# Performance work log

Measured on AMD Instinct MI355X. Metric: run time of the kernel, lower is better.

Reference implementation:

```python
import jax, jax.numpy as jnp
import numpy as np

CHANNELS = 256
REDUCTION = 4
REDUCED = max(1, CHANNELS // REDUCTION)  # 64


def setup_inputs() -> dict:
    key = jax.random.key(0)
    kx, kq, kk, kv, ko = jax.random.split(key, 5)
    B, C, H, W = 4, CHANNELS, 48, 48
    x = jax.random.normal(kx, (B, C, H, W), dtype=jnp.float32)
    # 1x1 conv weights (bias=False) for 3 q/k/v branches, stored as [3, reduced, C]
    wq = jax.random.normal(kq, (3, REDUCED, C), dtype=jnp.float32) * 0.05
    wk = jax.random.normal(kk, (3, REDUCED, C), dtype=jnp.float32) * 0.05
    wv = jax.random.normal(kv, (3, REDUCED, C), dtype=jnp.float32) * 0.05
    # output 1x1 conv: [C, 3*reduced]
    wo = jax.random.normal(ko, (C, 3 * REDUCED), dtype=jnp.float32) * 0.05
    return {"x": x, "wq": wq, "wk": wk, "wv": wv, "wo": wo}


def reference(x, wq, wk, wv, wo):
    B, C, H, W = x.shape
    N = H * W
    r = wq.shape[1]
    scale = 1.0 / float(r) ** 0.5
    xf = x.reshape(B, C, N)                      # [B, C, N]
    # 1x1 convs == channel matmuls; all 3 branches at once
    qs = jnp.einsum('irc,bcn->ibrn', wq, xf)     # [3, B, r, N]
    ks = jnp.einsum('irc,bcn->ibrn', wk, xf)
    vs = jnp.einsum('irc,bcn->ibrn', wv, xf)
    outs = []
    for i in range(3):                           # structural 3x3 nesting
        q = qs[i]                                # [B, r, N]
        acc = jnp.zeros((B, r, N), dtype=x.dtype)
        for j in range(3):
            # attn[b, n, m] = softmax_m(q[b,:,n] . k[b,:,m] / sqrt(r))
            attn = jax.nn.softmax(jnp.einsum('brn,brm->bnm', q, ks[j]) * scale, axis=-1)
            acc = acc + jnp.einsum('brm,bnm->brn', vs[j], attn)
        outs.append(acc)
    combined = jnp.concatenate(outs, axis=1)     # [B, 3r, N]
    out = jnp.einsum('cr,brn->bcn', wo, combined).reshape(B, C, H, W)
    return x * jax.nn.sigmoid(out)
```

## Files before the change

kernel.cpp:

```cpp
#include <hip/hip_runtime.h>


#define BB 4
#define CC 256
#define NN_ 2304
#define RR 64

#define OQ 0
#define OK_ 1769472
#define OV 3538944
#define OC 5308416
#define CSTR 1769472
#define FR_IB 147456
#define OXF 10616832
#define OWF 12976128
#define OWOF 13123584

typedef __bf16 bf16x8 __attribute__((ext_vector_type(8)));
typedef float f32x16 __attribute__((ext_vector_type(16)));
typedef unsigned short ushort8 __attribute__((ext_vector_type(8)));
typedef unsigned int uintx2 __attribute__((ext_vector_type(2)));
typedef unsigned int uintx4 __attribute__((ext_vector_type(4)));

#if __has_builtin(__builtin_amdgcn_exp2f)
#define EXP2(x) __builtin_amdgcn_exp2f(x)
#else
#define EXP2(x) exp2f(x)
#endif

__device__ __forceinline__ float bf2f(unsigned short s) {
    unsigned int u = ((unsigned int)s) << 16;
    return __builtin_bit_cast(float, u);
}
__device__ __forceinline__ unsigned int pk_bf16(float lo, float hi) {
    unsigned int r;
    asm("v_cvt_pk_bf16_f32 %0, %1, %2" : "=v"(r) : "v"(lo), "v"(hi));
    return r;
}

__global__ __launch_bounds__(256) void prep_kernel(
    const float* __restrict__ x, const float* __restrict__ wq,
    const float* __restrict__ wk, const float* __restrict__ wv,
    const float* __restrict__ wo, unsigned short* __restrict__ wsb)
{
    int bid = blockIdx.x;
    int t = threadIdx.x;
    if (bid < 9) {
        int s = bid;
        int type = s / 3, i = s % 3;
        const float* wsel = (type == 0) ? wq : (type == 1 ? wk : wv);
        const float scale = (type == 0) ? 0.18033688011112042f : 1.0f;
        unsigned short* dst = wsb + OWF + s * 16384;
        #pragma unroll
        for (int p = 0; p < 8; ++p) {
            int u = t + 256 * p;
            int ks = u >> 7, rb = (u >> 6) & 1, lo = u & 63;
            int row = rb * 32 + (lo & 31), c = ks * 16 + 8 * (lo >> 5);
            const float* src = wsel + ((i * 64 + row) * 256 + c);
            float4 f0 = *(const float4*)(src);
            float4 f1 = *(const float4*)(src + 4);
            uintx4 pwv = {pk_bf16(f0.x * scale, f0.y * scale),
                          pk_bf16(f0.z * scale, f0.w * scale),
                          pk_bf16(f1.x * scale, f1.y * scale),
                          pk_bf16(f1.z * scale, f1.w * scale)};
            *(uintx4*)(dst + (ks * 2 + rb) * 512 + lo * 8) = pwv;
        }
        return;
    }
    if (bid < 12) {
        int bb = bid - 9;
        #pragma unroll
        for (int p = 0; p < 8; ++p) {
            int u = t + 256 * p;
            int cg = bb * 32 + (u >> 6);
            int lane = u & 63;
            int ks = cg >> 3, rb = cg & 7;
            int row = rb * 32 + (lane & 31);
            int g = ks * 16 + 8 * (lane >> 5);
            const float* src = wo + row * 192 + g;
            float4 f0 = *(const float4*)(src);
            float4 f1 = *(const float4*)(src + 4);
            uintx4 pwv = {pk_bf16(f0.x, f0.y), pk_bf16(f0.z, f0.w),
                          pk_bf16(f1.x, f1.y), pk_bf16(f1.z, f1.w)};
            *(uintx4*)(wsb + OWOF + cg * 512 + lane * 8) = pwv;
        }
        return;
    }
    __shared__ __align__(16) float xs[64 * 132];
    int xb = bid - 12;
    int cq  = xb & 3;
    int nt2 = (xb >> 2) % 18;
    int b   = xb / 72;
    int c0 = cq * 64, n0 = nt2 * 128;
    #pragma unroll
    for (int p = 0; p < 8; ++p) {
        int u = t + 256 * p;
        int cl = u >> 5, nq = (u & 31) * 4;
        *(float4*)&xs[cl * 132 + nq] =
            *(const float4*)&x[((size_t)(b * CC + c0 + cl)) * NN_ + n0 + nq];
    }
    __syncthreads();
    unsigned short* xfb = wsb + OXF + ((size_t)b) * 72 * 16 * 512;
    #pragma unroll
    for (int p = 0; p < 4; ++p) {
        int u = t + 256 * p;
        int nb_l = u >> 8, ks_l = (u >> 6) & 3, lo = u & 63;
        int hh = lo >> 5, idx = lo & 31;
        int clb = ks_l * 16 + 8 * hh;
        int nn = nb_l * 32 + idx;
        unsigned int pw[4];
        #pragma unroll
        for (int d = 0; d < 4; ++d) {
            float a  = xs[(clb + 2 * d) * 132 + nn];
            float bb2 = xs[(clb + 2 * d + 1) * 132 + nn];
            pw[d] = pk_bf16(a, bb2);
        }
        int nb = nt2 * 4 + nb_l, ks = cq * 4 + ks_l;
        *(uintx4*)(xfb + (nb * 16 + ks) * 512 + lo * 8) =
            (uintx4){pw[0], pw[1], pw[2], pw[3]};
    }
}

__global__ __launch_bounds__(256) void proj_mfma(unsigned short* __restrict__ wsb)
{
    int bid = blockIdx.x;
    int s = bid / 72;
    int rem = bid % 72;
    int b = rem / 18, nb4 = rem % 18;
    int type = s / 3, i = s % 3;
    int t = threadIdx.x;
    int w = t >> 6, lane = t & 63;
    int lq = lane & 31, h = lane >> 5;
    int nb = nb4 * 4 + w;

    const unsigned short* wf = wsb + OWF + s * 16384 + lane * 8;
    const unsigned short* xf = wsb + OXF + ((size_t)(b * 72 + nb) * 16) * 512 + lane * 8;

    f32x16 o0 = {}, o1 = {};
    if (type < 2) {
        #pragma unroll
        for (int ks = 0; ks < 16; ++ks) {
            bf16x8 a0 = *(const bf16x8*)(wf + ks * 1024);
            bf16x8 a1 = *(const bf16x8*)(wf + ks * 1024 + 512);
            bf16x8 bx = *(const bf16x8*)(xf + ks * 512);
            o0 = __builtin_amdgcn_mfma_f32_32x32x16_bf16(a0, bx, o0, 0, 0, 0);
            o1 = __builtin_amdgcn_mfma_f32_32x32x16_bf16(a1, bx, o1, 0, 0, 0);
        }
    } else {
        #pragma unroll
        for (int ks = 0; ks < 16; ++ks) {
            bf16x8 a0 = *(const bf16x8*)(wf + ks * 1024);
            bf16x8 a1 = *(const bf16x8*)(wf + ks * 1024 + 512);
            bf16x8 bx = *(const bf16x8*)(xf + ks * 512);
            o0 = __builtin_amdgcn_mfma_f32_32x32x16_bf16(bx, a0, o0, 0, 0, 0);
            o1 = __builtin_amdgcn_mfma_f32_32x32x16_bf16(bx, a1, o1, 0, 0, 0);
        }
    }

    unsigned short* dstbase =
        wsb + ((type == 0) ? OQ : (type == 1 ? OK_ : OV)) +
        ((size_t)(i * 4 + b)) * FR_IB + nb * 2048;

    if (type < 2) {
        #pragma unroll
        for (int g = 0; g < 4; ++g) {
            int kd = 8 * g + 4 * h;
            int off = (kd >> 4) * 512 + ((kd >> 3) & 1) * 256 + lq * 8 + (kd & 7);
            *(uintx2*)(dstbase + off) =
                (uintx2){pk_bf16(o0[4 * g], o0[4 * g + 1]),
                         pk_bf16(o0[4 * g + 2], o0[4 * g + 3])};
            int kd2 = kd + 32;
            int off2 = (kd2 >> 4) * 512 + ((kd2 >> 3) & 1) * 256 + lq * 8 + (kd2 & 7);
            *(uintx2*)(dstbase + off2) =
                (uintx2){pk_bf16(o1[4 * g], o1[4 * g + 1]),
                         pk_bf16(o1[4 * g + 2], o1[4 * g + 3])};
        }
    } else {
        #pragma unroll
        for (int g = 0; g < 4; ++g) {
            int off = (g >> 1) * 1024 + (g & 1) * 256 + lq * 8 + 4 * h;
            *(uintx2*)(dstbase + off) =
                (uintx2){pk_bf16(o0[4 * g], o0[4 * g + 1]),
                         pk_bf16(o0[4 * g + 2], o0[4 * g + 3])};
            *(uintx2*)(dstbase + off + 512) =
                (uintx2){pk_bf16(o1[4 * g], o1[4 * g + 1]),
                         pk_bf16(o1[4 * g + 2], o1[4 * g + 3])};
        }
    }
}

__global__ __launch_bounds__(256, 4) void attn_kernel(unsigned short* __restrict__ wsb)
{
    __shared__ __align__(16) float fl[4352];

    int bid = blockIdx.x;
    int wid = (bid & 7) * 162 + (bid >> 3);
    int s12 = wid / 108;
    int rem = wid % 108;
    int j = s12 >> 2, b = s12 & 3;
    int i = rem / 36;
    int qp = rem % 36;
    int w = threadIdx.x >> 6;
    int ks = w & 1, qloc = w >> 1;
    int lane = threadIdx.x & 63;
    int lq = lane & 31;
    int h = lane >> 5;
    int q0 = (qp * 2 + qloc) * 32;
    int nt = q0 >> 5;

    const unsigned short* qtf = wsb + OQ + ((size_t)(i * 4 + b)) * FR_IB +
                                nt * 2048 + lane * 8;
    const unsigned short* kp = wsb + OK_ + ((size_t)(j * 4 + b)) * FR_IB +
                               (size_t)(ks * 36) * 2048 + lane * 8;
    const unsigned short* vp = wsb + OV + ((size_t)(j * 4 + b)) * FR_IB +
                               (size_t)(ks * 36) * 2048 + lane * 8;

    bf16x8 bq0 = *(const bf16x8*)(qtf + 0);
    bf16x8 bq1 = *(const bf16x8*)(qtf + 512);
    bf16x8 bq2 = *(const bf16x8*)(qtf + 1024);
    bf16x8 bq3 = *(const bf16x8*)(qtf + 1536);

    f32x16 o0 = {}, o1 = {};
    float l_loc = 0.f;

    auto compute_step = [&](bf16x8 k0, bf16x8 k1, bf16x8 k2, bf16x8 k3,
                            int step) {
        const unsigned short* vb = vp + (size_t)step * 2048;
        bf16x8 v00 = *(const bf16x8*)(vb + 0 * 512);
        bf16x8 v10 = *(const bf16x8*)(vb + 1 * 512);
        bf16x8 v01 = *(const bf16x8*)(vb + 2 * 512);
        bf16x8 v11 = *(const bf16x8*)(vb + 3 * 512);

        f32x16 s = {};
        s = __builtin_amdgcn_mfma_f32_32x32x16_bf16(k0, bq0, s, 0, 0, 0);
        s = __builtin_amdgcn_mfma_f32_32x32x16_bf16(k1, bq1, s, 0, 0, 0);
        s = __builtin_amdgcn_mfma_f32_32x32x16_bf16(k2, bq2, s, 0, 0, 0);
        s = __builtin_amdgcn_mfma_f32_32x32x16_bf16(k3, bq3, s, 0, 0, 0);

        #pragma unroll
        for (int r = 0; r < 16; ++r) s[r] = EXP2(s[r]);
        l_loc += ((s[0] + s[1]) + (s[2] + s[3])) + ((s[4] + s[5]) + (s[6] + s[7])) +
                 ((s[8] + s[9]) + (s[10] + s[11])) + ((s[12] + s[13]) + (s[14] + s[15]));

        {
            unsigned int a0 = pk_bf16(s[0], s[1]);
            unsigned int a1 = pk_bf16(s[2], s[3]);
            unsigned int b0 = pk_bf16(s[4], s[5]);
            unsigned int b1 = pk_bf16(s[6], s[7]);
            uintx2 r0 = __builtin_amdgcn_permlane32_swap(a0, b0, false, false);
            uintx2 r1 = __builtin_amdgcn_permlane32_swap(a1, b1, false, false);
            uintx4 pwv = {r0[0], r1[0], r0[1], r1[1]};
            bf16x8 pa = __builtin_bit_cast(bf16x8, pwv);
            o0 = __builtin_amdgcn_mfma_f32_32x32x16_bf16(v00, pa, o0, 0, 0, 0);
            o1 = __builtin_amdgcn_mfma_f32_32x32x16_bf16(v10, pa, o1, 0, 0, 0);
        }
        {
            unsigned int a0 = pk_bf16(s[8], s[9]);
            unsigned int a1 = pk_bf16(s[10], s[11]);
            unsigned int b0 = pk_bf16(s[12], s[13]);
            unsigned int b1 = pk_bf16(s[14], s[15]);
            uintx2 r0 = __builtin_amdgcn_permlane32_swap(a0, b0, false, false);
            uintx2 r1 = __builtin_amdgcn_permlane32_swap(a1, b1, false, false);
            uintx4 pwv = {r0[0], r1[0], r0[1], r1[1]};
            bf16x8 pa = __builtin_bit_cast(bf16x8, pwv);
            o0 = __builtin_amdgcn_mfma_f32_32x32x16_bf16(v01, pa, o0, 0, 0, 0);
            o1 = __builtin_amdgcn_mfma_f32_32x32x16_bf16(v11, pa, o1, 0, 0, 0);
        }
    };

    bf16x8 kA0 = *(const bf16x8*)(kp + 0 * 512);
    bf16x8 kA1 = *(const bf16x8*)(kp + 1 * 512);
    bf16x8 kA2 = *(const bf16x8*)(kp + 2 * 512);
    bf16x8 kA3 = *(const bf16x8*)(kp + 3 * 512);

    for (int step = 0; step < 36; step += 2) {
        const unsigned short* kbB = kp + (size_t)(step + 1) * 2048;
        bf16x8 kB0 = *(const bf16x8*)(kbB + 0 * 512);
        bf16x8 kB1 = *(const bf16x8*)(kbB + 1 * 512);
        bf16x8 kB2 = *(const bf16x8*)(kbB + 2 * 512);
        bf16x8 kB3 = *(const bf16x8*)(kbB + 3 * 512);

        compute_step(kA0, kA1, kA2, kA3, step);

        int nx = (step + 2 < 36) ? (step + 2) : 0;
        const unsigned short* kbA = kp + (size_t)nx * 2048;
        kA0 = *(const bf16x8*)(kbA + 0 * 512);
        kA1 = *(const bf16x8*)(kbA + 1 * 512);
        kA2 = *(const bf16x8*)(kbA + 2 * 512);
        kA3 = *(const bf16x8*)(kbA + 3 * 512);

        compute_step(kB0, kB1, kB2, kB3, step + 1);
    }

    float l_full = l_loc + __shfl_xor(l_loc, 32);

    int off = qloc * 2112;
    if (ks == 1) {
        #pragma unroll
        for (int reg = 0; reg < 16; ++reg) {
            fl[off + reg * 64 + lane] = o0[reg];
            fl[off + 1024 + reg * 64 + lane] = o1[reg];
        }
        fl[off + 2048 + lane] = l_full;
    }
    __syncthreads();
    if (ks == 1) return;

    #pragma unroll
    for (int reg = 0; reg < 16; ++reg) {
        o0[reg] += fl[off + reg * 64 + lane];
        o1[reg] += fl[off + 1024 + reg * 64 + lane];
    }
    float l_tot = l_full + fl[off + 2048 + lane];
    __syncthreads();

    float inv = 1.f / l_tot;
    o0 *= inv; o1 *= inv;

    float* tw = fl + qloc * 2080;
    #pragma unroll
    for (int reg = 0; reg < 16; ++reg) {
        int rv = (reg & 3) + 8 * (reg >> 2) + 4 * h;
        tw[lq * 65 + rv] = o0[reg];
        tw[lq * 65 + 32 + rv] = o1[reg];
    }
    unsigned short* cb = wsb + OC + (size_t)j * CSTR +
                         ((size_t)((b * 72 + nt) * 12 + i * 4)) * 512;
    #pragma unroll
    for (int ksl = 0; ksl < 4; ++ksl) {
        const float* src = tw + lq * 65 + ksl * 16 + 8 * h;
        uintx4 pwv = {pk_bf16(src[0], src[1]), pk_bf16(src[2], src[3]),
                      pk_bf16(src[4], src[5]), pk_bf16(src[6], src[7])};
        *(uintx4*)(cb + ksl * 512 + lane * 8) = pwv;
    }
}

__global__ __launch_bounds__(256) void out_mfma(
    const float* __restrict__ x, const unsigned short* __restrict__ wsb,
    float* __restrict__ out)
{
    int bid = blockIdx.x;
    int ch = bid & 1;
    int nt = (bid >> 1) % 72;
    int b  = bid / 144;
    int n0 = nt * 32;
    int t = threadIdx.x;
    int w = t >> 6, lane = t & 63;
    int lq = lane & 31, h = lane >> 5;
    int rb = ch * 4 + w;

    const unsigned short* wof = wsb + OWOF + lane * 8;
    const unsigned short* cbase = wsb + OC +
        ((size_t)((b * 72 + nt) * 12)) * 512 + lane * 8;

    f32x16 acc = {};
    #pragma unroll
    for (int j = 0; j < 3; ++j) {
        const unsigned short* cj = cbase + (size_t)j * CSTR;
        #pragma unroll
        for (int ksx = 0; ksx < 12; ++ksx) {
            bf16x8 bx = *(const bf16x8*)(cj + ksx * 512);
            bf16x8 a0 = *(const bf16x8*)(wof + (ksx * 8 + rb) * 512);
            acc = __builtin_amdgcn_mfma_f32_32x32x16_bf16(a0, bx, acc, 0, 0, 0);
        }
    }

    int c0 = rb * 32;
    #pragma unroll
    for (int reg = 0; reg < 16; ++reg) {
        int c = c0 + (reg & 3) + 8 * (reg >> 2) + 4 * h;
        size_t idx = ((size_t)(b * CC + c)) * NN_ + n0 + lq;
        float sg = 1.f / (1.f + EXP2(acc[reg] * -1.44269504f));
        out[idx] = x[idx] * sg;
    }
}

extern "C" void kernel_launch(void* const* d_in, const int* in_sizes, int n_in,
                              void* d_out, int out_size, void* d_ws, size_t ws_size,
                              hipStream_t stream) {
    const float* x  = (const float*)d_in[0];
    const float* wq = (const float*)d_in[1];
    const float* wk = (const float*)d_in[2];
    const float* wv = (const float*)d_in[3];
    const float* wo = (const float*)d_in[4];
    unsigned short* wsb = (unsigned short*)d_ws;
    float* out = (float*)d_out;

    prep_kernel<<<300, 256, 0, stream>>>(x, wq, wk, wv, wo, wsb);
    proj_mfma<<<648, 256, 0, stream>>>(wsb);
    attn_kernel<<<1296, 256, 0, stream>>>(wsb);
    out_mfma<<<576, 256, 0, stream>>>(x, wsb, out);
}
```

Baseline: 96.70 us.

## Split attention key range four ways per query tile with tree reduction

Each attention block now handles a single 32-query tile, with its four waves each covering a quarter of the keys. Previously each block handled two query tiles, with two waves splitting the keys. The grid doubles to 2592 blocks. Partial outputs and softmax denominators are combined through a two-level shared-memory tree reduction. This raises parallelism and shortens each wave's serial loop, at the cost of an extra barrier, more reduction traffic, and Q fragments reloaded by twice as many blocks.

```diff
diff --git a/kernel.cpp b/kernel.cpp
--- a/kernel.cpp
+++ b/kernel.cpp
@@ -191,29 +191,27 @@
 
 __global__ __launch_bounds__(256, 4) void attn_kernel(unsigned short* __restrict__ wsb)
 {
-    __shared__ __align__(16) float fl[4352];
+    __shared__ __align__(16) float fl[4224];
 
     int bid = blockIdx.x;
-    int wid = (bid & 7) * 162 + (bid >> 3);
-    int s12 = wid / 108;
-    int rem = wid % 108;
+    int wid = (bid & 7) * 324 + (bid >> 3);
+    int s12 = wid / 216;
+    int rem = wid % 216;
     int j = s12 >> 2, b = s12 & 3;
-    int i = rem / 36;
-    int qp = rem % 36;
+    int i = rem / 72;
+    int qp = rem % 72;
     int w = threadIdx.x >> 6;
-    int ks = w & 1, qloc = w >> 1;
     int lane = threadIdx.x & 63;
     int lq = lane & 31;
     int h = lane >> 5;
-    int q0 = (qp * 2 + qloc) * 32;
-    int nt = q0 >> 5;
+    int q0 = qp * 32;
 
     const unsigned short* qtf = wsb + OQ + ((size_t)(i * 4 + b)) * FR_IB +
-                                nt * 2048 + lane * 8;
+                                qp * 2048 + lane * 8;
     const unsigned short* kp = wsb + OK_ + ((size_t)(j * 4 + b)) * FR_IB +
-                               (size_t)(ks * 36) * 2048 + lane * 8;
+                               (size_t)(w * 18) * 2048 + lane * 8;
     const unsigned short* vp = wsb + OV + ((size_t)(j * 4 + b)) * FR_IB +
-                               (size_t)(ks * 36) * 2048 + lane * 8;
+                               (size_t)(w * 18) * 2048 + lane * 8;
 
     bf16x8 bq0 = *(const bf16x8*)(qtf + 0);
     bf16x8 bq1 = *(const bf16x8*)(qtf + 512);
@@ -273,7 +271,7 @@
     bf16x8 kA2 = *(const bf16x8*)(kp + 2 * 512);
     bf16x8 kA3 = *(const bf16x8*)(kp + 3 * 512);
 
-    for (int step = 0; step < 36; step += 2) {
+    for (int step = 0; step < 18; step += 2) {
         const unsigned short* kbB = kp + (size_t)(step + 1) * 2048;
         bf16x8 kB0 = *(const bf16x8*)(kbB + 0 * 512);
         bf16x8 kB1 = *(const bf16x8*)(kbB + 1 * 512);
@@ -282,7 +280,7 @@
 
         compute_step(kA0, kA1, kA2, kA3, step);
 
-        int nx = (step + 2 < 36) ? (step + 2) : 0;
+        int nx = (step + 2 < 18) ? (step + 2) : 0;
         const unsigned short* kbA = kp + (size_t)nx * 2048;
         kA0 = *(const bf16x8*)(kbA + 0 * 512);
         kA1 = *(const bf16x8*)(kbA + 1 * 512);
@@ -294,30 +292,49 @@
 
     float l_full = l_loc + __shfl_xor(l_loc, 32);
 
-    int off = qloc * 2112;
-    if (ks == 1) {
+    if (w & 1) {
+        float* sl = fl + (w >> 1) * 2112;
         #pragma unroll
         for (int reg = 0; reg < 16; ++reg) {
-            fl[off + reg * 64 + lane] = o0[reg];
-            fl[off + 1024 + reg * 64 + lane] = o1[reg];
-        }
-        fl[off + 2048 + lane] = l_full;
+            sl[reg * 64 + lane] = o0[reg];
+            sl[1024 + reg * 64 + lane] = o1[reg];
+        }
+        sl[2048 + lane] = l_full;
     }
     __syncthreads();
-    if (ks == 1) return;
+    if (!(w & 1)) {
+        const float* sl = fl + (w >> 1) * 2112;
+        #pragma unroll
+        for (int reg = 0; reg < 16; ++reg) {
+            o0[reg] += sl[reg * 64 + lane];
+            o1[reg] += sl[1024 + reg * 64 + lane];
+        }
+        l_full += sl[2048 + lane];
+    }
+    __syncthreads();
+    if (w == 2) {
+        float* sl = fl;
+        #pragma unroll
+        for (int reg = 0; reg < 16; ++reg) {
+            sl[reg * 64 + lane] = o0[reg];
+            sl[1024 + reg * 64 + lane] = o1[reg];
+        }
+        sl[2048 + lane] = l_full;
+    }
+    __syncthreads();
+    if (w != 0) return;
 
     #pragma unroll
     for (int reg = 0; reg < 16; ++reg) {
-        o0[reg] += fl[off + reg * 64 + lane];
-        o1[reg] += fl[off + 1024 + reg * 64 + lane];
-    }
-    float l_tot = l_full + fl[off + 2048 + lane];
-    __syncthreads();
-
-    float inv = 1.f / l_tot;
+        o0[reg] += fl[reg * 64 + lane];
+        o1[reg] += fl[1024 + reg * 64 + lane];
+    }
+    l_full += fl[2048 + lane];
+
+    float inv = 1.f / l_full;
     o0 *= inv; o1 *= inv;
 
-    float* tw = fl + qloc * 2080;
+    float* tw = fl;
     #pragma unroll
     for (int reg = 0; reg < 16; ++reg) {
         int rv = (reg & 3) + 8 * (reg >> 2) + 4 * h;
@@ -325,7 +342,7 @@
         tw[lq * 65 + 32 + rv] = o1[reg];
     }
     unsigned short* cb = wsb + OC + (size_t)j * CSTR +
-                         ((size_t)((b * 72 + nt) * 12 + i * 4)) * 512;
+                         ((size_t)((b * 72 + qp) * 12 + i * 4)) * 512;
     #pragma unroll
     for (int ksl = 0; ksl < 4; ++ksl) {
         const float* src = tw + lq * 65 + ksl * 16 + 8 * h;
@@ -388,6 +405,6 @@
 
     prep_kernel<<<300, 256, 0, stream>>>(x, wq, wk, wv, wo, wsb);
     proj_mfma<<<648, 256, 0, stream>>>(wsb);
-    attn_kernel<<<1296, 256, 0, stream>>>(wsb);
+    attn_kernel<<<2592, 256, 0, stream>>>(wsb);
     out_mfma<<<576, 256, 0, stream>>>(x, wsb, out);
 }
```

New measurement: 96.15 us. No clear change (-0.6%).
